# Kernel optimization log

Measured on AMD Instinct MI355X. Metric: run time of the kernel, lower is better.

The kernel has to match this reference:

```python
import jax, jax.numpy as jnp
import numpy as np

N_USERS = 100_000
N_ITEMS = 50_000
N = N_USERS + N_ITEMS
N_LAYERS = 3
ALPHA = 0.8
D = 64
IMG_D = 4096
TXT_D = 384
N_INTER = 2_000_000  # user-item interactions; symmetric nnz = 2*N_INTER


def setup_inputs() -> dict:
    # --- build symmetric-normalized bipartite adjacency (D^-1/2 A D^-1/2) in numpy ---
    rng = np.random.default_rng(0)
    u = rng.integers(0, N_USERS, N_INTER).astype(np.int32)
    i = (rng.integers(0, N_ITEMS, N_INTER) + N_USERS).astype(np.int32)
    rows = np.concatenate([u, i])
    cols = np.concatenate([i, u])
    deg = np.bincount(rows, minlength=N).astype(np.float32)
    d_inv = np.where(deg > 0, deg ** -0.5, 0.0).astype(np.float32)
    vals = d_inv[rows] * d_inv[cols]

    key = jax.random.key(0)
    ks = jax.random.split(key, 8)
    xav_img = float(np.sqrt(6.0 / (IMG_D + D)))
    xav_txt = float(np.sqrt(6.0 / (TXT_D + D)))
    return {
        "image_feats": jax.random.normal(ks[0], (N_ITEMS, IMG_D), jnp.float32),
        "text_feats": jax.random.normal(ks[1], (N_ITEMS, TXT_D), jnp.float32),
        "image_pref": jax.random.normal(ks[2], (N_USERS, D), jnp.float32),
        "text_pref": jax.random.normal(ks[3], (N_USERS, D), jnp.float32),
        "W_img": jax.random.uniform(ks[4], (IMG_D, D), jnp.float32, -xav_img, xav_img),
        "b_img": jnp.zeros((D,), jnp.float32),
        "W_txt": jax.random.uniform(ks[5], (TXT_D, D), jnp.float32, -xav_txt, xav_txt),
        "b_txt": jnp.zeros((D,), jnp.float32),
        "adj_vals": jnp.asarray(vals),
        "adj_rows": jnp.asarray(rows),
        "adj_cols": jnp.asarray(cols),
    }


def _spmm(rows, cols, vals, x):
    # sparse COO @ dense: out[r] += vals[e] * x[cols[e]]
    return jax.ops.segment_sum(vals[:, None] * x[cols], rows, num_segments=N)


def _l2norm(x):
    # F.normalize(x, dim=1): row-wise L2 with eps clamp
    return x / jnp.clip(jnp.linalg.norm(x, axis=1, keepdims=True), 1e-12)


def reference(image_feats, text_feats, image_pref, text_pref,
              W_img, b_img, W_txt, b_txt, adj_vals, adj_rows, adj_cols):
    img = _l2norm(image_feats @ W_img + b_img)   # [n_items, D]
    txt = _l2norm(text_feats @ W_txt + b_txt)    # [n_items, D]
    ego_i = jnp.concatenate([image_pref, img], axis=0)  # [N, D]
    ego_t = jnp.concatenate([text_pref, txt], axis=0)   # [N, D]
    for _ in range(N_LAYERS):
        ego_i = _spmm(adj_rows, adj_cols, adj_vals, ego_i) + ALPHA * ego_i
        ego_t = _spmm(adj_rows, adj_cols, adj_vals, ego_t) + ALPHA * ego_t
    user_preference = jnp.concatenate([ego_i[:N_USERS], ego_t[:N_USERS]], axis=1)  # [n_users, 2D]
    items = jnp.concatenate([ego_i[N_USERS:], ego_t[N_USERS:]], axis=1)            # [n_items, 2D]
    return user_preference, items
```

## Files before the change

### kernel.cpp

```cpp
#include <hip/hip_runtime.h>
#include <hip/hip_bf16.h>

#define N_USERS 100000
#define N_ITEMS 50000
#define N_TOTAL 150000
#define NNZ     4000000
#define ALPHA_F 0.8f
#define ELL_CAP 128
#define KCHUNK  128

#define C_COPY 512
#define C_SCAT 1024

typedef __attribute__((ext_vector_type(8))) short bf16x8;
typedef __attribute__((ext_vector_type(4))) float f32x4;

static __device__ __forceinline__ short f2bf(float f) {
    unsigned u = __builtin_bit_cast(unsigned, f);
    unsigned r = (u + 0x7fff + ((u >> 16) & 1)) >> 16;
    return (short)r;
}
static __device__ __forceinline__ unsigned pack_bf2(float a, float b) {
    return (unsigned)(unsigned short)f2bf(a) | ((unsigned)(unsigned short)f2bf(b) << 16);
}
static __device__ __forceinline__ float bf_lo(unsigned u) { return __uint_as_float(u << 16); }
static __device__ __forceinline__ float bf_hi(unsigned u) { return __uint_as_float(u & 0xFFFF0000u); }

static __device__ __forceinline__ void gload_lds16(const void* src, void* dst) {
    __builtin_amdgcn_global_load_lds(
        (const __attribute__((address_space(1))) unsigned*)src,
        (__attribute__((address_space(3))) unsigned*)dst, 16, 0, 0);
}


__global__ __launch_bounds__(256) void prep_kernel(const float* __restrict__ Wimg,
                                                   const float* __restrict__ Wtxt,
                                                   int* __restrict__ cnt,
                                                   short* __restrict__ Wti,
                                                   short* __restrict__ Wtt) {
    const int T0 = N_TOTAL;
    const int T1 = T0 + 4096 * 64;
    const int T2 = T1 + 384 * 64;
    int i = blockIdx.x * 256 + threadIdx.x;
    int stride = gridDim.x * 256;
    for (; i < T2; i += stride) {
        if (i < T0) {
            cnt[i] = 0;
        } else if (i < T1) {
            int idx = i - T0; int k = idx >> 6, n = idx & 63;
            Wti[(size_t)n * 4096 + k] = f2bf(Wimg[(size_t)k * 64 + n]);
        } else {
            int idx = i - T1; int k = idx >> 6, n = idx & 63;
            Wtt[(size_t)n * 384 + k] = f2bf(Wtxt[(size_t)k * 64 + n]);
        }
    }
}


__global__ __launch_bounds__(256) void scat_copy_kernel(
        const int* __restrict__ rows, const int* __restrict__ cols,
        const float* __restrict__ vals, int* __restrict__ cnt, int2* __restrict__ ell,
        const float* __restrict__ img_pref, const float* __restrict__ txt_pref,
        unsigned* __restrict__ egob) {
    int b = blockIdx.x;
    if (b < C_COPY) {
        int idx = b * 256 + threadIdx.x;
        int stride = C_COPY * 256;
        for (; idx < N_USERS * 16; idx += stride) {
            int row = idx >> 4, w4 = (idx & 15) << 2;
            float4 iv = *reinterpret_cast<const float4*>(&img_pref[(size_t)row * 64 + w4]);
            float4 tv = *reinterpret_cast<const float4*>(&txt_pref[(size_t)row * 64 + w4]);
            uint4 m;
            m.x = pack_bf2(iv.x, tv.x); m.y = pack_bf2(iv.y, tv.y);
            m.z = pack_bf2(iv.z, tv.z); m.w = pack_bf2(iv.w, tv.w);
            *reinterpret_cast<uint4*>(&egob[(size_t)row * 64 + w4]) = m;
        }
    } else {
        int i = (b - C_COPY) * 256 + threadIdx.x;
        int stride = C_SCAT * 256;
        for (; i < NNZ; i += stride) {
            int r = rows[i];
            int p = atomicAdd(&cnt[r], 1);
            if (p < ELL_CAP)
                ell[(size_t)r * ELL_CAP + p] = make_int2(cols[i], __float_as_int(vals[i]));
        }
    }
}


static __device__ __forceinline__ void compute_chunk(
        const float* at, const short* bt, int wave, int lane,
        f32x4& c0, f32x4& c1, f32x4& c2, f32x4& c3) {
    const int col = lane & 15, kb = lane >> 4;
    const int arow = 16 * wave + col;
    const int aswz = (col & 7) << 4;
    const int bswz = col << 4;
    const char* abase = (const char*)at + arow * 512;
    const char* bbase = (const char*)bt + col * 256;
    #pragma unroll
    for (int ks = 0; ks < 4; ++ks) {
        int Xa = ks * 128 + kb * 32;
        float4 a0v = *(const float4*)(abase + ((Xa)      ^ aswz));
        float4 a1v = *(const float4*)(abase + ((Xa + 16) ^ aswz));
        bf16x8 af;
        af[0]=f2bf(a0v.x); af[1]=f2bf(a0v.y); af[2]=f2bf(a0v.z); af[3]=f2bf(a0v.w);
        af[4]=f2bf(a1v.x); af[5]=f2bf(a1v.y); af[6]=f2bf(a1v.z); af[7]=f2bf(a1v.w);
        int xb = (ks * 64 + kb * 16) ^ bswz;
        bf16x8 b0 = *(const bf16x8*)(bbase + xb);
        bf16x8 b1 = *(const bf16x8*)(bbase + 16 * 256 + xb);
        bf16x8 b2 = *(const bf16x8*)(bbase + 32 * 256 + xb);
        bf16x8 b3 = *(const bf16x8*)(bbase + 48 * 256 + xb);
        c0 = __builtin_amdgcn_mfma_f32_16x16x32_bf16(af, b0, c0, 0, 0, 0);
        c1 = __builtin_amdgcn_mfma_f32_16x16x32_bf16(af, b1, c1, 0, 0, 0);
        c2 = __builtin_amdgcn_mfma_f32_16x16x32_bf16(af, b2, c2, 0, 0, 0);
        c3 = __builtin_amdgcn_mfma_f32_16x16x32_bf16(af, b3, c3, 0, 0, 0);
    }
}

__global__ __launch_bounds__(256) void gemm_lds_kernel(
        const float* __restrict__ Aimg, const float* __restrict__ Atxt,
        const short* __restrict__ Wti, const short* __restrict__ Wtt,
        const float* __restrict__ bimg, const float* __restrict__ btxt,
        unsigned* __restrict__ egob_items) {
    __shared__ __align__(16) float atile[2][64 * KCHUNK];
    __shared__ __align__(16) short btile[2][64 * KCHUNK];
    const int t = threadIdx.x;
    const int wave = t >> 6, lane = t & 63;
    const int col = lane & 15, kb = lane >> 4;
    const int row0 = blockIdx.x * 64;
    const int gmax = N_ITEMS - 1;

    const int s_arow  = 16 * wave + (lane >> 5);
    const int s_axoff = (lane & 31) * 16;
    const int s_bcol  = 16 * wave + (lane >> 4);
    const int s_bxoff = (lane & 15) * 16;

    auto stageA = [&](const float* A, int K, int k0, int bi) {
        #pragma unroll
        for (int c = 0; c < 8; ++c) {
            int r = s_arow + 2 * c;
            int gr = row0 + r; gr = gr > gmax ? gmax : gr;
            int sw = (r & 7) << 4;
            const char* src = (const char*)A + ((size_t)gr * K + k0) * 4 + (s_axoff ^ sw);
            char* dst = (char*)&atile[bi][0] + r * 512 + s_axoff;
            gload_lds16(src, dst);
        }
    };
    auto stageB = [&](const short* W, int K, int k0, int bi) {
        #pragma unroll
        for (int c = 0; c < 4; ++c) {
            int bc = s_bcol + 4 * c;
            int sw = (bc & 15) << 4;
            const char* src = (const char*)W + ((size_t)bc * K + k0) * 2 + (s_bxoff ^ sw);
            char* dst = (char*)&btile[bi][0] + bc * 256 + s_bxoff;
            gload_lds16(src, dst);
        }
    };

    f32x4 z = {0.f, 0.f, 0.f, 0.f};
    f32x4 ai0 = z, ai1 = z, ai2 = z, ai3 = z;
    f32x4 at0 = z, at1 = z, at2 = z, at3 = z;

    stageA(Aimg, 4096, 0, 0); stageB(Wti, 4096, 0, 0);
    asm volatile("s_waitcnt vmcnt(0)" ::: "memory");
    __syncthreads();
    for (int ch = 0; ch < 32; ++ch) {
        int bi = ch & 1;
        if (ch + 1 < 32) {
            stageA(Aimg, 4096, (ch + 1) * KCHUNK, bi ^ 1);
            stageB(Wti, 4096, (ch + 1) * KCHUNK, bi ^ 1);
        }
        compute_chunk(&atile[bi][0], &btile[bi][0], wave, lane, ai0, ai1, ai2, ai3);
        asm volatile("s_waitcnt vmcnt(0)" ::: "memory");
        __syncthreads();
    }
    stageA(Atxt, 384, 0, 0); stageB(Wtt, 384, 0, 0);
    asm volatile("s_waitcnt vmcnt(0)" ::: "memory");
    __syncthreads();
    for (int ch = 0; ch < 3; ++ch) {
        int bi = ch & 1;
        if (ch + 1 < 3) {
            stageA(Atxt, 384, (ch + 1) * KCHUNK, bi ^ 1);
            stageB(Wtt, 384, (ch + 1) * KCHUNK, bi ^ 1);
        }
        compute_chunk(&atile[bi][0], &btile[bi][0], wave, lane, at0, at1, at2, at3);
        asm volatile("s_waitcnt vmcnt(0)" ::: "memory");
        __syncthreads();
    }

    float bi0 = bimg[ 0 + col], bi1 = bimg[16 + col], bi2 = bimg[32 + col], bi3 = bimg[48 + col];
    float bt0 = btxt[ 0 + col], bt1 = btxt[16 + col], bt2 = btxt[32 + col], bt3 = btxt[48 + col];
    #pragma unroll
    for (int i = 0; i < 4; ++i) {
        ai0[i] += bi0; ai1[i] += bi1; ai2[i] += bi2; ai3[i] += bi3;
        at0[i] += bt0; at1[i] += bt1; at2[i] += bt2; at3[i] += bt3;
    }
    #pragma unroll
    for (int i = 0; i < 4; ++i) {
        float ssi = ai0[i]*ai0[i] + ai1[i]*ai1[i] + ai2[i]*ai2[i] + ai3[i]*ai3[i];
        float sst = at0[i]*at0[i] + at1[i]*at1[i] + at2[i]*at2[i] + at3[i]*at3[i];
        #pragma unroll
        for (int off = 1; off < 16; off <<= 1) {
            ssi += __shfl_xor(ssi, off, 64);
            sst += __shfl_xor(sst, off, 64);
        }
        float rni = 1.0f / fmaxf(sqrtf(ssi), 1e-12f);
        float rnt = 1.0f / fmaxf(sqrtf(sst), 1e-12f);
        int r = row0 + 16 * wave + kb * 4 + i;
        if (r < N_ITEMS) {
            unsigned* ob = egob_items + (size_t)r * 64 + col;
            ob[ 0] = pack_bf2(ai0[i]*rni, at0[i]*rnt);
            ob[16] = pack_bf2(ai1[i]*rni, at1[i]*rnt);
            ob[32] = pack_bf2(ai2[i]*rni, at2[i]*rnt);
            ob[48] = pack_bf2(ai3[i]*rni, at3[i]*rnt);
        }
    }
}


__global__ __launch_bounds__(256) void sort_kernel(const int* __restrict__ cnt,
                                                   int2* __restrict__ ell) {
    int row = blockIdx.x * 4 + (threadIdx.x >> 6);
    if (row >= N_TOTAL) return;
    int lane = threadIdx.x & 63;
    int deg = min(cnt[row], ELL_CAP);
    if (deg <= 1) return;
    int2* base = ell + (size_t)row * ELL_CAP;
    int2 e0 = (lane < deg)      ? base[lane]      : make_int2(0x7FFFFFFF, 0);
    int2 e1 = (lane + 64 < deg) ? base[lane + 64] : make_int2(0x7FFFFFFF, 0);
    #pragma unroll
    for (int k = 2; k <= 128; k <<= 1) {
        #pragma unroll
        for (int j = 64; j >= 1; j >>= 1) {
            if (j >= k) continue;
            if (j == 64) {
                if (e0.x > e1.x) { int2 tmp = e0; e0 = e1; e1 = tmp; }
            } else {
                int2 p0, p1;
                p0.x = __shfl_xor(e0.x, j, 64); p0.y = __shfl_xor(e0.y, j, 64);
                p1.x = __shfl_xor(e1.x, j, 64); p1.y = __shfl_xor(e1.y, j, 64);
                bool up0 = ((lane & k) == 0);
                bool up1 = (((lane + 64) & k) == 0);
                bool lo0 = ((lane & j) == 0);
                bool keepmin0 = (up0 == lo0);
                bool keepmin1 = (up1 == lo0);
                if (keepmin0 ? (e0.x > p0.x) : (e0.x < p0.x)) e0 = p0;
                if (keepmin1 ? (e1.x > p1.x) : (e1.x < p1.x)) e1 = p1;
            }
        }
    }
    if (lane < deg)      base[lane]      = e0;
    if (lane + 64 < deg) base[lane + 64] = e1;
}


__global__ __launch_bounds__(256) void spmm_kernel(
        const int* __restrict__ cnt, const int2* __restrict__ ell,
        const unsigned* __restrict__ xb,
        float* __restrict__ out32, unsigned* __restrict__ outb) {
    int row = blockIdx.x * 4 + (threadIdx.x >> 6);
    if (row >= N_TOTAL) return;
    int lane = threadIdx.x & 63;
    unsigned sw = xb[(size_t)row * 64 + lane];
    float2 acc;
    acc.x = ALPHA_F * bf_lo(sw);
    acc.y = ALPHA_F * bf_hi(sw);
    int deg = min(cnt[row], ELL_CAP);
    const int2* base = ell + (size_t)row * ELL_CAP;
    int i = 0;
    for (; i + 8 <= deg; i += 8) {
        int4 p0 = *reinterpret_cast<const int4*>(base + i);
        int4 p1 = *reinterpret_cast<const int4*>(base + i + 2);
        int4 p2 = *reinterpret_cast<const int4*>(base + i + 4);
        int4 p3 = *reinterpret_cast<const int4*>(base + i + 6);
        unsigned g0 = xb[(size_t)p0.x * 64 + lane];
        unsigned g1 = xb[(size_t)p0.z * 64 + lane];
        unsigned g2 = xb[(size_t)p1.x * 64 + lane];
        unsigned g3 = xb[(size_t)p1.z * 64 + lane];
        unsigned g4 = xb[(size_t)p2.x * 64 + lane];
        unsigned g5 = xb[(size_t)p2.z * 64 + lane];
        unsigned g6 = xb[(size_t)p3.x * 64 + lane];
        unsigned g7 = xb[(size_t)p3.z * 64 + lane];
        float v0 = __int_as_float(p0.y), v1 = __int_as_float(p0.w);
        float v2 = __int_as_float(p1.y), v3 = __int_as_float(p1.w);
        float v4 = __int_as_float(p2.y), v5 = __int_as_float(p2.w);
        float v6 = __int_as_float(p3.y), v7 = __int_as_float(p3.w);
        acc.x = fmaf(v0, bf_lo(g0), acc.x); acc.y = fmaf(v0, bf_hi(g0), acc.y);
        acc.x = fmaf(v1, bf_lo(g1), acc.x); acc.y = fmaf(v1, bf_hi(g1), acc.y);
        acc.x = fmaf(v2, bf_lo(g2), acc.x); acc.y = fmaf(v2, bf_hi(g2), acc.y);
        acc.x = fmaf(v3, bf_lo(g3), acc.x); acc.y = fmaf(v3, bf_hi(g3), acc.y);
        acc.x = fmaf(v4, bf_lo(g4), acc.x); acc.y = fmaf(v4, bf_hi(g4), acc.y);
        acc.x = fmaf(v5, bf_lo(g5), acc.x); acc.y = fmaf(v5, bf_hi(g5), acc.y);
        acc.x = fmaf(v6, bf_lo(g6), acc.x); acc.y = fmaf(v6, bf_hi(g6), acc.y);
        acc.x = fmaf(v7, bf_lo(g7), acc.x); acc.y = fmaf(v7, bf_hi(g7), acc.y);
    }
    for (; i < deg; ++i) {
        int2 c = base[i];
        float v = __int_as_float(c.y);
        unsigned g = xb[(size_t)c.x * 64 + lane];
        acc.x = fmaf(v, bf_lo(g), acc.x);
        acc.y = fmaf(v, bf_hi(g), acc.y);
    }
    if (out32) {
        out32[(size_t)row * 128 + lane] = acc.x;
        out32[(size_t)row * 128 + 64 + lane] = acc.y;
    }
    if (outb)
        outb[(size_t)row * 64 + lane] = pack_bf2(acc.x, acc.y);
}


extern "C" void kernel_launch(void* const* d_in, const int* in_sizes, int n_in,
                              void* d_out, int out_size, void* d_ws, size_t ws_size,
                              hipStream_t stream) {
    const float* image_feats = (const float*)d_in[0];
    const float* text_feats  = (const float*)d_in[1];
    const float* image_pref  = (const float*)d_in[2];
    const float* text_pref   = (const float*)d_in[3];
    const float* W_img       = (const float*)d_in[4];
    const float* b_img       = (const float*)d_in[5];
    const float* W_txt       = (const float*)d_in[6];
    const float* b_txt       = (const float*)d_in[7];
    const float* adj_vals    = (const float*)d_in[8];
    const int*   adj_rows    = (const int*)d_in[9];
    const int*   adj_cols    = (const int*)d_in[10];

    float* out = (float*)d_out;

    char* ws = (char*)d_ws;
    size_t off = 0;
    auto alloc = [&](size_t bytes) { char* p = ws + off; off += (bytes + 255) & ~size_t(255); return p; };
    int*      cnt    = (int*)     alloc(N_TOTAL * sizeof(int));
    int2*     ell    = (int2*)    alloc((size_t)N_TOTAL * ELL_CAP * sizeof(int2));
    unsigned* m0     = (unsigned*)alloc((size_t)N_TOTAL * 64 * sizeof(unsigned));
    unsigned* m1     = (unsigned*)alloc((size_t)N_TOTAL * 64 * sizeof(unsigned));
    short*    Wt_img = (short*)   alloc((size_t)64 * 4096 * sizeof(short));
    short*    Wt_txt = (short*)   alloc((size_t)64 * 384 * sizeof(short));
    (void)ws_size; (void)out_size; (void)n_in; (void)in_sizes;

    prep_kernel<<<512, 256, 0, stream>>>(W_img, W_txt, cnt, Wt_img, Wt_txt);

    scat_copy_kernel<<<C_COPY + C_SCAT, 256, 0, stream>>>(
        adj_rows, adj_cols, adj_vals, cnt, ell, image_pref, text_pref, m0);

    unsigned* m0_items = m0 + (size_t)N_USERS * 64;
    gemm_lds_kernel<<<(N_ITEMS + 63) / 64, 256, 0, stream>>>(
        image_feats, text_feats, Wt_img, Wt_txt, b_img, b_txt, m0_items);

    const int ROW_GRID = (N_TOTAL + 3) / 4;
    sort_kernel<<<ROW_GRID, 256, 0, stream>>>(cnt, ell);

    spmm_kernel<<<ROW_GRID, 256, 0, stream>>>(cnt, ell, m0, nullptr, m1);
    spmm_kernel<<<ROW_GRID, 256, 0, stream>>>(cnt, ell, m1, nullptr, m0);
    spmm_kernel<<<ROW_GRID, 256, 0, stream>>>(cnt, ell, m0, out, nullptr);
}
```

Baseline: 1.141 ms.

## Fuse GEMM with scatter/copy kernel and sort into first SpMM

Merges the item-feature GEMM, the user-pref copy and the COO-to-ELL scatter into one launch with block-range dispatch, so the bandwidth-bound scatter overlaps the GEMM. The GEMM moves to 64-wide K chunks with a single continuous 70-chunk pipeline over image and text features, and uses a partial vmcnt wait so loads stay in flight across the barrier. The bitonic row sort is fused into the first SpMM, which reads the sorted neighbour list from LDS instead of rereading it from global memory. Costs include smaller chunks with more barriers, and different block types competing for CUs within the merged launch.

```diff
diff --git a/kernel.cpp b/kernel.cpp
--- a/kernel.cpp
+++ b/kernel.cpp
@@ -7,10 +7,12 @@
 #define NNZ     4000000
 #define ALPHA_F 0.8f
 #define ELL_CAP 128
-#define KCHUNK  128
-
-#define C_COPY 512
-#define C_SCAT 1024
+
+#define G_GEMM 782
+#define G_COPY 256
+#define G_SCAT 1024
+#define NC_IMG 64
+#define NC_ALL 70
 
 typedef __attribute__((ext_vector_type(8))) short bf16x8;
 typedef __attribute__((ext_vector_type(4))) float f32x4;
@@ -57,15 +59,135 @@
 }
 
 
-__global__ __launch_bounds__(256) void scat_copy_kernel(
+static __device__ __forceinline__ void compute_chunk(
+        const float* at, const short* bt, int wave, int lane,
+        f32x4& c0, f32x4& c1, f32x4& c2, f32x4& c3) {
+    const int col = lane & 15, kb = lane >> 4;
+    const int arow = 16 * wave + col;
+    const char* abase = (const char*)at + arow * 256;
+    const int aswz = (arow & 7) << 4;
+    const int bswz = (col & 7) << 4;
+    const char* bb = (const char*)bt;
+    #pragma unroll
+    for (int ks = 0; ks < 2; ++ks) {
+        int Xa = ks * 128 + kb * 32;
+        float4 a0v = *(const float4*)(abase + ((Xa)      ^ aswz));
+        float4 a1v = *(const float4*)(abase + ((Xa + 16) ^ aswz));
+        bf16x8 af;
+        af[0]=f2bf(a0v.x); af[1]=f2bf(a0v.y); af[2]=f2bf(a0v.z); af[3]=f2bf(a0v.w);
+        af[4]=f2bf(a1v.x); af[5]=f2bf(a1v.y); af[6]=f2bf(a1v.z); af[7]=f2bf(a1v.w);
+        int xb = (ks * 64 + kb * 16) ^ bswz;
+        bf16x8 b0 = *(const bf16x8*)(bb + (col +  0) * 128 + xb);
+        bf16x8 b1 = *(const bf16x8*)(bb + (col + 16) * 128 + xb);
+        bf16x8 b2 = *(const bf16x8*)(bb + (col + 32) * 128 + xb);
+        bf16x8 b3 = *(const bf16x8*)(bb + (col + 48) * 128 + xb);
+        c0 = __builtin_amdgcn_mfma_f32_16x16x32_bf16(af, b0, c0, 0, 0, 0);
+        c1 = __builtin_amdgcn_mfma_f32_16x16x32_bf16(af, b1, c1, 0, 0, 0);
+        c2 = __builtin_amdgcn_mfma_f32_16x16x32_bf16(af, b2, c2, 0, 0, 0);
+        c3 = __builtin_amdgcn_mfma_f32_16x16x32_bf16(af, b3, c3, 0, 0, 0);
+    }
+}
+
+
+__global__ __launch_bounds__(256) void mega_kernel(
+        const float* __restrict__ Aimg, const float* __restrict__ Atxt,
+        const short* __restrict__ Wti, const short* __restrict__ Wtt,
+        const float* __restrict__ bimg, const float* __restrict__ btxt,
+        unsigned* __restrict__ egob,
         const int* __restrict__ rows, const int* __restrict__ cols,
         const float* __restrict__ vals, int* __restrict__ cnt, int2* __restrict__ ell,
-        const float* __restrict__ img_pref, const float* __restrict__ txt_pref,
-        unsigned* __restrict__ egob) {
+        const float* __restrict__ img_pref, const float* __restrict__ txt_pref) {
+    __shared__ __align__(16) float atile[2][64 * 64];
+    __shared__ __align__(16) short btile[2][64 * 64];
     int b = blockIdx.x;
-    if (b < C_COPY) {
-        int idx = b * 256 + threadIdx.x;
-        int stride = C_COPY * 256;
+    int t = threadIdx.x;
+    int wave = t >> 6, lane = t & 63;
+    if (b < G_GEMM) {
+        const int row0 = b * 64;
+        const int gmax = N_ITEMS - 1;
+        const int col = lane & 15, kb = lane >> 4;
+
+        auto stageA = [&](const float* A, int K, int k0, int bi) {
+            #pragma unroll
+            for (int c = 0; c < 4; ++c) {
+                int g = c * 4 + wave;
+                int r = g * 4 + (lane >> 4);
+                int gr = row0 + r; gr = gr > gmax ? gmax : gr;
+                int boff = ((lane & 15) * 16) ^ ((r & 7) << 4);
+                const char* src = (const char*)A + ((size_t)gr * K + k0) * 4 + boff;
+                char* dst = (char*)&atile[bi][0] + g * 1024 + lane * 16;
+                gload_lds16(src, dst);
+            }
+        };
+        auto stageB = [&](const short* W, int K, int k0, int bi) {
+            #pragma unroll
+            for (int c = 0; c < 2; ++c) {
+                int g = c * 4 + wave;
+                int bc = g * 8 + (lane >> 3);
+                int boff = ((lane & 7) * 16) ^ ((bc & 7) << 4);
+                const char* src = (const char*)W + ((size_t)bc * K + k0) * 2 + boff;
+                char* dst = (char*)&btile[bi][0] + g * 1024 + lane * 16;
+                gload_lds16(src, dst);
+            }
+        };
+        auto stage = [&](int ci, int bi) {
+            if (ci < NC_IMG) { stageA(Aimg, 4096, ci * 64, bi); stageB(Wti, 4096, ci * 64, bi); }
+            else { stageA(Atxt, 384, (ci - NC_IMG) * 64, bi); stageB(Wtt, 384, (ci - NC_IMG) * 64, bi); }
+        };
+
+        f32x4 z = {0.f,0.f,0.f,0.f};
+        f32x4 ai0 = z, ai1 = z, ai2 = z, ai3 = z;
+        f32x4 at0 = z, at1 = z, at2 = z, at3 = z;
+
+        stage(0, 0);
+        for (int ci = 0; ci < NC_ALL; ++ci) {
+            int bi = ci & 1;
+            if (ci + 1 < NC_ALL) {
+                stage(ci + 1, bi ^ 1);
+                asm volatile("s_waitcnt vmcnt(6)" ::: "memory");
+            } else {
+                asm volatile("s_waitcnt vmcnt(0)" ::: "memory");
+            }
+            __builtin_amdgcn_s_barrier();
+            __builtin_amdgcn_sched_barrier(0);
+            if (ci < NC_IMG) compute_chunk(&atile[bi][0], &btile[bi][0], wave, lane, ai0, ai1, ai2, ai3);
+            else             compute_chunk(&atile[bi][0], &btile[bi][0], wave, lane, at0, at1, at2, at3);
+            asm volatile("" ::: "memory");
+            __builtin_amdgcn_s_barrier();
+            __builtin_amdgcn_sched_barrier(0);
+        }
+
+        float bi0 = bimg[ 0 + col], bi1 = bimg[16 + col], bi2 = bimg[32 + col], bi3 = bimg[48 + col];
+        float bt0 = btxt[ 0 + col], bt1 = btxt[16 + col], bt2 = btxt[32 + col], bt3 = btxt[48 + col];
+        #pragma unroll
+        for (int i = 0; i < 4; ++i) {
+            ai0[i] += bi0; ai1[i] += bi1; ai2[i] += bi2; ai3[i] += bi3;
+            at0[i] += bt0; at1[i] += bt1; at2[i] += bt2; at3[i] += bt3;
+        }
+        unsigned* egob_items = egob + (size_t)N_USERS * 64;
+        #pragma unroll
+        for (int i = 0; i < 4; ++i) {
+            float ssi = ai0[i]*ai0[i] + ai1[i]*ai1[i] + ai2[i]*ai2[i] + ai3[i]*ai3[i];
+            float sst = at0[i]*at0[i] + at1[i]*at1[i] + at2[i]*at2[i] + at3[i]*at3[i];
+            #pragma unroll
+            for (int off = 1; off < 16; off <<= 1) {
+                ssi += __shfl_xor(ssi, off, 64);
+                sst += __shfl_xor(sst, off, 64);
+            }
+            float rni = 1.0f / fmaxf(sqrtf(ssi), 1e-12f);
+            float rnt = 1.0f / fmaxf(sqrtf(sst), 1e-12f);
+            int r = row0 + 16 * wave + kb * 4 + i;
+            if (r < N_ITEMS) {
+                unsigned* ob = egob_items + (size_t)r * 64 + col;
+                ob[ 0] = pack_bf2(ai0[i]*rni, at0[i]*rnt);
+                ob[16] = pack_bf2(ai1[i]*rni, at1[i]*rnt);
+                ob[32] = pack_bf2(ai2[i]*rni, at2[i]*rnt);
+                ob[48] = pack_bf2(ai3[i]*rni, at3[i]*rnt);
+            }
+        }
+    } else if (b < G_GEMM + G_COPY) {
+        int idx = (b - G_GEMM) * 256 + t;
+        int stride = G_COPY * 256;
         for (; idx < N_USERS * 16; idx += stride) {
             int row = idx >> 4, w4 = (idx & 15) << 2;
             float4 iv = *reinterpret_cast<const float4*>(&img_pref[(size_t)row * 64 + w4]);
@@ -76,8 +198,8 @@
             *reinterpret_cast<uint4*>(&egob[(size_t)row * 64 + w4]) = m;
         }
     } else {
-        int i = (b - C_COPY) * 256 + threadIdx.x;
-        int stride = C_SCAT * 256;
+        int i = (b - G_GEMM - G_COPY) * 256 + t;
+        int stride = G_SCAT * 256;
         for (; i < NNZ; i += stride) {
             int r = rows[i];
             int p = atomicAdd(&cnt[r], 1);
@@ -88,146 +210,22 @@
 }
 
 
-static __device__ __forceinline__ void compute_chunk(
-        const float* at, const short* bt, int wave, int lane,
-        f32x4& c0, f32x4& c1, f32x4& c2, f32x4& c3) {
-    const int col = lane & 15, kb = lane >> 4;
-    const int arow = 16 * wave + col;
-    const int aswz = (col & 7) << 4;
-    const int bswz = col << 4;
-    const char* abase = (const char*)at + arow * 512;
-    const char* bbase = (const char*)bt + col * 256;
-    #pragma unroll
-    for (int ks = 0; ks < 4; ++ks) {
-        int Xa = ks * 128 + kb * 32;
-        float4 a0v = *(const float4*)(abase + ((Xa)      ^ aswz));
-        float4 a1v = *(const float4*)(abase + ((Xa + 16) ^ aswz));
-        bf16x8 af;
-        af[0]=f2bf(a0v.x); af[1]=f2bf(a0v.y); af[2]=f2bf(a0v.z); af[3]=f2bf(a0v.w);
-        af[4]=f2bf(a1v.x); af[5]=f2bf(a1v.y); af[6]=f2bf(a1v.z); af[7]=f2bf(a1v.w);
-        int xb = (ks * 64 + kb * 16) ^ bswz;
-        bf16x8 b0 = *(const bf16x8*)(bbase + xb);
-        bf16x8 b1 = *(const bf16x8*)(bbase + 16 * 256 + xb);
-        bf16x8 b2 = *(const bf16x8*)(bbase + 32 * 256 + xb);
-        bf16x8 b3 = *(const bf16x8*)(bbase + 48 * 256 + xb);
-        c0 = __builtin_amdgcn_mfma_f32_16x16x32_bf16(af, b0, c0, 0, 0, 0);
-        c1 = __builtin_amdgcn_mfma_f32_16x16x32_bf16(af, b1, c1, 0, 0, 0);
-        c2 = __builtin_amdgcn_mfma_f32_16x16x32_bf16(af, b2, c2, 0, 0, 0);
-        c3 = __builtin_amdgcn_mfma_f32_16x16x32_bf16(af, b3, c3, 0, 0, 0);
-    }
-}
-
-__global__ __launch_bounds__(256) void gemm_lds_kernel(
-        const float* __restrict__ Aimg, const float* __restrict__ Atxt,
-        const short* __restrict__ Wti, const short* __restrict__ Wtt,
-        const float* __restrict__ bimg, const float* __restrict__ btxt,
-        unsigned* __restrict__ egob_items) {
-    __shared__ __align__(16) float atile[2][64 * KCHUNK];
-    __shared__ __align__(16) short btile[2][64 * KCHUNK];
-    const int t = threadIdx.x;
-    const int wave = t >> 6, lane = t & 63;
-    const int col = lane & 15, kb = lane >> 4;
-    const int row0 = blockIdx.x * 64;
-    const int gmax = N_ITEMS - 1;
-
-    const int s_arow  = 16 * wave + (lane >> 5);
-    const int s_axoff = (lane & 31) * 16;
-    const int s_bcol  = 16 * wave + (lane >> 4);
-    const int s_bxoff = (lane & 15) * 16;
-
-    auto stageA = [&](const float* A, int K, int k0, int bi) {
-        #pragma unroll
-        for (int c = 0; c < 8; ++c) {
-            int r = s_arow + 2 * c;
-            int gr = row0 + r; gr = gr > gmax ? gmax : gr;
-            int sw = (r & 7) << 4;
-            const char* src = (const char*)A + ((size_t)gr * K + k0) * 4 + (s_axoff ^ sw);
-            char* dst = (char*)&atile[bi][0] + r * 512 + s_axoff;
-            gload_lds16(src, dst);
-        }
-    };
-    auto stageB = [&](const short* W, int K, int k0, int bi) {
-        #pragma unroll
-        for (int c = 0; c < 4; ++c) {
-            int bc = s_bcol + 4 * c;
-            int sw = (bc & 15) << 4;
-            const char* src = (const char*)W + ((size_t)bc * K + k0) * 2 + (s_bxoff ^ sw);
-            char* dst = (char*)&btile[bi][0] + bc * 256 + s_bxoff;
-            gload_lds16(src, dst);
-        }
-    };
-
-    f32x4 z = {0.f, 0.f, 0.f, 0.f};
-    f32x4 ai0 = z, ai1 = z, ai2 = z, ai3 = z;
-    f32x4 at0 = z, at1 = z, at2 = z, at3 = z;
-
-    stageA(Aimg, 4096, 0, 0); stageB(Wti, 4096, 0, 0);
-    asm volatile("s_waitcnt vmcnt(0)" ::: "memory");
-    __syncthreads();
-    for (int ch = 0; ch < 32; ++ch) {
-        int bi = ch & 1;
-        if (ch + 1 < 32) {
-            stageA(Aimg, 4096, (ch + 1) * KCHUNK, bi ^ 1);
-            stageB(Wti, 4096, (ch + 1) * KCHUNK, bi ^ 1);
-        }
-        compute_chunk(&atile[bi][0], &btile[bi][0], wave, lane, ai0, ai1, ai2, ai3);
-        asm volatile("s_waitcnt vmcnt(0)" ::: "memory");
-        __syncthreads();
-    }
-    stageA(Atxt, 384, 0, 0); stageB(Wtt, 384, 0, 0);
-    asm volatile("s_waitcnt vmcnt(0)" ::: "memory");
-    __syncthreads();
-    for (int ch = 0; ch < 3; ++ch) {
-        int bi = ch & 1;
-        if (ch + 1 < 3) {
-            stageA(Atxt, 384, (ch + 1) * KCHUNK, bi ^ 1);
-            stageB(Wtt, 384, (ch + 1) * KCHUNK, bi ^ 1);
-        }
-        compute_chunk(&atile[bi][0], &btile[bi][0], wave, lane, at0, at1, at2, at3);
-        asm volatile("s_waitcnt vmcnt(0)" ::: "memory");
-        __syncthreads();
-    }
-
-    float bi0 = bimg[ 0 + col], bi1 = bimg[16 + col], bi2 = bimg[32 + col], bi3 = bimg[48 + col];
-    float bt0 = btxt[ 0 + col], bt1 = btxt[16 + col], bt2 = btxt[32 + col], bt3 = btxt[48 + col];
-    #pragma unroll
-    for (int i = 0; i < 4; ++i) {
-        ai0[i] += bi0; ai1[i] += bi1; ai2[i] += bi2; ai3[i] += bi3;
-        at0[i] += bt0; at1[i] += bt1; at2[i] += bt2; at3[i] += bt3;
-    }
-    #pragma unroll
-    for (int i = 0; i < 4; ++i) {
-        float ssi = ai0[i]*ai0[i] + ai1[i]*ai1[i] + ai2[i]*ai2[i] + ai3[i]*ai3[i];
-        float sst = at0[i]*at0[i] + at1[i]*at1[i] + at2[i]*at2[i] + at3[i]*at3[i];
-        #pragma unroll
-        for (int off = 1; off < 16; off <<= 1) {
-            ssi += __shfl_xor(ssi, off, 64);
-            sst += __shfl_xor(sst, off, 64);
-        }
-        float rni = 1.0f / fmaxf(sqrtf(ssi), 1e-12f);
-        float rnt = 1.0f / fmaxf(sqrtf(sst), 1e-12f);
-        int r = row0 + 16 * wave + kb * 4 + i;
-        if (r < N_ITEMS) {
-            unsigned* ob = egob_items + (size_t)r * 64 + col;
-            ob[ 0] = pack_bf2(ai0[i]*rni, at0[i]*rnt);
-            ob[16] = pack_bf2(ai1[i]*rni, at1[i]*rnt);
-            ob[32] = pack_bf2(ai2[i]*rni, at2[i]*rnt);
-            ob[48] = pack_bf2(ai3[i]*rni, at3[i]*rnt);
-        }
-    }
-}
-
-
-__global__ __launch_bounds__(256) void sort_kernel(const int* __restrict__ cnt,
-                                                   int2* __restrict__ ell) {
-    int row = blockIdx.x * 4 + (threadIdx.x >> 6);
-    if (row >= N_TOTAL) return;
-    int lane = threadIdx.x & 63;
-    int deg = min(cnt[row], ELL_CAP);
-    if (deg <= 1) return;
-    int2* base = ell + (size_t)row * ELL_CAP;
-    int2 e0 = (lane < deg)      ? base[lane]      : make_int2(0x7FFFFFFF, 0);
-    int2 e1 = (lane + 64 < deg) ? base[lane + 64] : make_int2(0x7FFFFFFF, 0);
+__global__ __launch_bounds__(256) void spmm_sort_kernel(
+        const int* __restrict__ cnt, int2* __restrict__ ell,
+        const unsigned* __restrict__ xb, unsigned* __restrict__ outb) {
+    __shared__ __align__(16) int2 srt[4][ELL_CAP];
+    int wid = threadIdx.x >> 6, lane = threadIdx.x & 63;
+    int row = blockIdx.x * 4 + wid;
+    bool valid = row < N_TOTAL;
+    int deg = 0;
+    int2* base = nullptr;
+    int2 e0 = make_int2(0x7FFFFFFF, 0), e1 = e0;
+    if (valid) {
+        deg = min(cnt[row], ELL_CAP);
+        base = ell + (size_t)row * ELL_CAP;
+        if (lane < deg)      e0 = base[lane];
+        if (lane + 64 < deg) e1 = base[lane + 64];
+    }
     #pragma unroll
     for (int k = 2; k <= 128; k <<= 1) {
         #pragma unroll
@@ -249,8 +247,54 @@
             }
         }
     }
-    if (lane < deg)      base[lane]      = e0;
-    if (lane + 64 < deg) base[lane + 64] = e1;
+    if (valid) {
+        if (lane < deg)      base[lane]      = e0;
+        if (lane + 64 < deg) base[lane + 64] = e1;
+    }
+    srt[wid][lane] = e0;
+    srt[wid][lane + 64] = e1;
+    __syncthreads();
+    if (!valid) return;
+    unsigned sw = xb[(size_t)row * 64 + lane];
+    float2 acc;
+    acc.x = ALPHA_F * bf_lo(sw);
+    acc.y = ALPHA_F * bf_hi(sw);
+    const int2* s = srt[wid];
+    int i = 0;
+    for (; i + 8 <= deg; i += 8) {
+        int4 p0 = *reinterpret_cast<const int4*>(s + i);
+        int4 p1 = *reinterpret_cast<const int4*>(s + i + 2);
+        int4 p2 = *reinterpret_cast<const int4*>(s + i + 4);
+        int4 p3 = *reinterpret_cast<const int4*>(s + i + 6);
+        unsigned g0 = xb[(size_t)p0.x * 64 + lane];
+        unsigned g1 = xb[(size_t)p0.z * 64 + lane];
+        unsigned g2 = xb[(size_t)p1.x * 64 + lane];
+        unsigned g3 = xb[(size_t)p1.z * 64 + lane];
+        unsigned g4 = xb[(size_t)p2.x * 64 + lane];
+        unsigned g5 = xb[(size_t)p2.z * 64 + lane];
+        unsigned g6 = xb[(size_t)p3.x * 64 + lane];
+        unsigned g7 = xb[(size_t)p3.z * 64 + lane];
+        float v0 = __int_as_float(p0.y), v1 = __int_as_float(p0.w);
+        float v2 = __int_as_float(p1.y), v3 = __int_as_float(p1.w);
+        float v4 = __int_as_float(p2.y), v5 = __int_as_float(p2.w);
+        float v6 = __int_as_float(p3.y), v7 = __int_as_float(p3.w);
+        acc.x = fmaf(v0, bf_lo(g0), acc.x); acc.y = fmaf(v0, bf_hi(g0), acc.y);
+        acc.x = fmaf(v1, bf_lo(g1), acc.x); acc.y = fmaf(v1, bf_hi(g1), acc.y);
+        acc.x = fmaf(v2, bf_lo(g2), acc.x); acc.y = fmaf(v2, bf_hi(g2), acc.y);
+        acc.x = fmaf(v3, bf_lo(g3), acc.x); acc.y = fmaf(v3, bf_hi(g3), acc.y);
+        acc.x = fmaf(v4, bf_lo(g4), acc.x); acc.y = fmaf(v4, bf_hi(g4), acc.y);
+        acc.x = fmaf(v5, bf_lo(g5), acc.x); acc.y = fmaf(v5, bf_hi(g5), acc.y);
+        acc.x = fmaf(v6, bf_lo(g6), acc.x); acc.y = fmaf(v6, bf_hi(g6), acc.y);
+        acc.x = fmaf(v7, bf_lo(g7), acc.x); acc.y = fmaf(v7, bf_hi(g7), acc.y);
+    }
+    for (; i < deg; ++i) {
+        int2 c = s[i];
+        float v = __int_as_float(c.y);
+        unsigned g = xb[(size_t)c.x * 64 + lane];
+        acc.x = fmaf(v, bf_lo(g), acc.x);
+        acc.y = fmaf(v, bf_hi(g), acc.y);
+    }
+    outb[(size_t)row * 64 + lane] = pack_bf2(acc.x, acc.y);
 }
 
 
@@ -340,17 +384,12 @@
 
     prep_kernel<<<512, 256, 0, stream>>>(W_img, W_txt, cnt, Wt_img, Wt_txt);
 
-    scat_copy_kernel<<<C_COPY + C_SCAT, 256, 0, stream>>>(
-        adj_rows, adj_cols, adj_vals, cnt, ell, image_pref, text_pref, m0);
-
-    unsigned* m0_items = m0 + (size_t)N_USERS * 64;
-    gemm_lds_kernel<<<(N_ITEMS + 63) / 64, 256, 0, stream>>>(
-        image_feats, text_feats, Wt_img, Wt_txt, b_img, b_txt, m0_items);
+    mega_kernel<<<G_GEMM + G_COPY + G_SCAT, 256, 0, stream>>>(
+        image_feats, text_feats, Wt_img, Wt_txt, b_img, b_txt, m0,
+        adj_rows, adj_cols, adj_vals, cnt, ell, image_pref, text_pref);
 
     const int ROW_GRID = (N_TOTAL + 3) / 4;
-    sort_kernel<<<ROW_GRID, 256, 0, stream>>>(cnt, ell);
-
-    spmm_kernel<<<ROW_GRID, 256, 0, stream>>>(cnt, ell, m0, nullptr, m1);
+    spmm_sort_kernel<<<ROW_GRID, 256, 0, stream>>>(cnt, ell, m0, m1);
     spmm_kernel<<<ROW_GRID, 256, 0, stream>>>(cnt, ell, m1, nullptr, m0);
     spmm_kernel<<<ROW_GRID, 256, 0, stream>>>(cnt, ell, m0, out, nullptr);
 }
```

After: 995.7 us. 12.7% less time.
